# Optimization experiments

Measured on AMD Instinct MI355X. Metric: run time of the kernel, lower is better.

Reference implementation:

```python
import jax, jax.numpy as jnp
import numpy as np

EPS = 1e-12
FP8_MAX = 448.0  # torch.finfo(float8_e4m3fn).max
G = 128  # tile/block group size


def per_tile_quant_dequant(x):
    # x: [seq, din]; one scale per 1x128 tile along din (per_tile_quant semantics)
    s, d = x.shape
    xt = x.reshape(s, d // G, G)
    amax = jnp.max(jnp.abs(xt), axis=-1, keepdims=True)
    scale = jnp.maximum(amax, EPS) / FP8_MAX
    q = jnp.clip(xt / scale, -FP8_MAX, FP8_MAX).astype(jnp.float8_e4m3fn)
    return (q.astype(jnp.float32) * scale).reshape(s, d)


def per_block_quant_dequant(w):
    # w: [ne, dout, din]; one scale per 128x128 block
    ne, dout, din = w.shape
    wb = w.reshape(ne, dout // G, G, din // G, G)
    amax = jnp.max(jnp.abs(wb), axis=(2, 4), keepdims=True)
    scale = jnp.maximum(amax, EPS) / FP8_MAX
    q = jnp.clip(wb / scale, -FP8_MAX, FP8_MAX).astype(jnp.float8_e4m3fn)
    return (q.astype(jnp.float32) * scale).reshape(ne, dout, din)


def grouped_gemm(xq, wq, tokens_per_expert):
    # xq: [seq, din] (tokens contiguous per expert); wq: [ne, dout, din]
    seq = xq.shape[0]
    ne, dout, _ = wq.shape
    ends = jnp.cumsum(tokens_per_expert)
    starts = ends - tokens_per_expert
    tok = jnp.arange(seq)
    out = jnp.zeros((seq, dout), dtype=jnp.float32)
    for e in range(ne):  # small fixed expert count
        mask = ((tok >= starts[e]) & (tok < ends[e]))[:, None]
        xe = jnp.where(mask, xq, 0.0)
        out = out + xe @ wq[e].T
    return out


def setup_inputs() -> dict:
    key = jax.random.key(0)
    k1, k2 = jax.random.split(key)
    ne, dout, din, seq = 8, 2048, 2048, 8192
    x = jax.random.normal(k1, (seq, din), dtype=jnp.float32)
    # weight stored flat as (ne*dout, din), as in the module
    weight = jax.random.normal(k2, (ne * dout, din), dtype=jnp.float32) * 0.02
    tokens_per_expert = jnp.full((ne,), seq // ne, dtype=jnp.int32)
    return {"input": x, "weight": weight, "tokens_per_expert": tokens_per_expert}


def reference(input, weight, tokens_per_expert):
    ne, dout, din = 8, 2048, 2048
    w = weight.reshape(ne, dout, din)
    xq = per_tile_quant_dequant(input)          # per-tile fp8 activation quant
    wq = per_block_quant_dequant(w)             # per-block fp8 weight quant
    return grouped_gemm(xq, wq, tokens_per_expert)
```

## Files before the change

kernel.cpp:

```cpp
#include <hip/hip_runtime.h>
#include <hip/hip_bf16.h>
#include <stdint.h>

#define NE   8
#define DOUT 2048
#define DIN  2048
#define SEQ  8192
#define GSZ  128
#define FP8_MAX 448.0f
#define EPSQ 1e-12f

typedef float f32x4  __attribute__((ext_vector_type(4)));
typedef float f32x16 __attribute__((ext_vector_type(16)));
typedef int   i32x4  __attribute__((ext_vector_type(4)));
typedef int   i32x8  __attribute__((ext_vector_type(8)));

__device__ __forceinline__ void async16(void* lds_base, const void* gptr) {
    __builtin_amdgcn_global_load_lds(
        (const __attribute__((address_space(1))) unsigned int*)gptr,
        (__attribute__((address_space(3))) unsigned int*)lds_base,
        16, 0, 0);
}

__global__ __launch_bounds__(256) void quant_x_kernel(
    const float* __restrict__ x, unsigned char* __restrict__ qx,
    float* __restrict__ sx)
{
    const int g = blockIdx.x * 256 + threadIdx.x;
    const float4 v = ((const float4*)x)[g];
    float a = fmaxf(fmaxf(fabsf(v.x), fabsf(v.y)),
                    fmaxf(fabsf(v.z), fabsf(v.w)));
    #pragma unroll
    for (int o = 16; o; o >>= 1) a = fmaxf(a, __shfl_xor(a, o));
    const float scale = fmaxf(a, EPSQ) / FP8_MAX;
    const int tile = g >> 5;
    if ((threadIdx.x & 31) == 0) sx[tile] = scale;

    float q0 = fminf(fmaxf(v.x / scale, -FP8_MAX), FP8_MAX);
    float q1 = fminf(fmaxf(v.y / scale, -FP8_MAX), FP8_MAX);
    float q2 = fminf(fmaxf(v.z / scale, -FP8_MAX), FP8_MAX);
    float q3 = fminf(fmaxf(v.w / scale, -FP8_MAX), FP8_MAX);
    int lo = __builtin_amdgcn_cvt_pk_fp8_f32(q0, q1, 0, false);
    int pk = __builtin_amdgcn_cvt_pk_fp8_f32(q2, q3, lo, true);
    ((unsigned int*)qx)[g] = (unsigned int)pk;
}

__global__ __launch_bounds__(256) void quant_w_kernel(
    const float* __restrict__ w, unsigned char* __restrict__ qw,
    float* __restrict__ sw)
{
    __shared__ float buf[128 * 128];
    __shared__ float red[4];

    const int cb = blockIdx.x;
    const int rb = blockIdx.y;
    const int e  = blockIdx.z;
    const int t  = threadIdx.x;
    const int lane = t & 63, wv = t >> 6;

    const size_t base = ((size_t)e * DOUT + rb * GSZ) * DIN + cb * GSZ;
    const float* wp = w + base;

    #pragma unroll
    for (int j = 0; j < 16; ++j) {
        int f16 = (wv * 16 + j) * 64 + lane;
        int row = f16 >> 5, cc = f16 & 31;
        async16(buf + (wv * 16 + j) * 256,
                wp + (size_t)row * DIN + cc * 4);
    }
    __syncthreads();

    float a = 0.f;
    #pragma unroll
    for (int i = 0; i < 16; ++i) {
        f32x4 v = *(const f32x4*)(buf + (t + i * 256) * 4);
        a = fmaxf(a, fmaxf(fmaxf(fabsf(v[0]), fabsf(v[1])),
                           fmaxf(fabsf(v[2]), fabsf(v[3]))));
    }
    #pragma unroll
    for (int o = 32; o; o >>= 1) a = fmaxf(a, __shfl_xor(a, o));
    if (lane == 0) red[wv] = a;
    __syncthreads();
    a = fmaxf(fmaxf(red[0], red[1]), fmaxf(red[2], red[3]));
    const float scale = fmaxf(a, EPSQ) / FP8_MAX;
    if (t == 0) sw[(e * 16 + rb) * 16 + cb] = scale;

    unsigned int* qout = (unsigned int*)(qw + base);
    #pragma unroll
    for (int i = 0; i < 16; ++i) {
        int idx = t + i * 256;
        f32x4 v = *(const f32x4*)(buf + idx * 4);
        float q0 = fminf(fmaxf(v[0] / scale, -FP8_MAX), FP8_MAX);
        float q1 = fminf(fmaxf(v[1] / scale, -FP8_MAX), FP8_MAX);
        float q2 = fminf(fmaxf(v[2] / scale, -FP8_MAX), FP8_MAX);
        float q3 = fminf(fmaxf(v[3] / scale, -FP8_MAX), FP8_MAX);
        int lo = __builtin_amdgcn_cvt_pk_fp8_f32(q0, q1, 0, false);
        int pk = __builtin_amdgcn_cvt_pk_fp8_f32(q2, q3, lo, true);
        int r = idx >> 5, c4 = idx & 31;
        qout[r * (DIN / 4) + c4] = (unsigned int)pk;
    }
}

__global__ __launch_bounds__(512, 2) void gemm_kernel(
    const unsigned char* __restrict__ qx, const float* __restrict__ sx,
    const unsigned char* __restrict__ qw, const float* __restrict__ sw,
    const int* __restrict__ tpe, float* __restrict__ out)
{
    __shared__ __align__(16) unsigned char Asm[2][256 * 128];
    __shared__ __align__(16) unsigned char Bsm[2][256 * 128];
    __shared__ __align__(16) float Rs[16 * 256];
    __shared__ __align__(16) float SwL[2 * 16];

    const int tid  = threadIdx.x;
    const int lane = tid & 63;
    const int wv   = tid >> 6;
    const int wm   = wv >> 2;
    const int wn   = wv & 3;
    const int l31  = lane & 31;
    const int h    = lane >> 5;
    const int nh   = wn >> 1;

    const int lid  = blockIdx.x;
    const int xcd  = lid & 7, t8 = lid >> 3;
    const int mbid = xcd * 4 + (t8 >> 3);
    const int nb   = t8 & 7;
    const int r0   = mbid * 256, n0 = nb * 256;

    int e = -1, start = 0;
    #pragma unroll
    for (int i = 0; i < NE; ++i) {
        int end = start + tpe[i];
        if (r0 >= start && r0 < end) e = i;
        start = end;
    }
    if (e < 0) {
        f32x4 z = {0.f, 0.f, 0.f, 0.f};
        for (int i = tid; i < 256 * 64; i += 512) {
            int r = i >> 6, c4 = i & 63;
            *(f32x4*)(out + (size_t)(r0 + r) * DOUT + n0 + c4 * 4) = z;
        }
        return;
    }

    for (int i = tid; i < 16 * 256; i += 512) {
        int row = i >> 4, kb = i & 15;
        const float* sp = sx + (size_t)(r0 + row) * 16;
        Rs[kb * 256 + row] = (kb == 0) ? sp[15] : sp[kb - 1] / sp[kb];
    }
    if (tid < 32) {
        int nhh = tid >> 4, kb = tid & 15;
        const float* wp = sw + ((e * 16) + (nb * 2 + nhh)) * 16;
        SwL[nhh * 16 + kb] = (kb == 0) ? wp[15] : wp[kb - 1] / wp[kb];
    }

    const unsigned char* Ag = qx + (size_t)r0 * DIN;
    const unsigned char* Bg = qw + (size_t)e * DOUT * DIN + (size_t)n0 * DIN;

    int soff[4], ldst[4];
    #pragma unroll
    for (int j = 0; j < 4; ++j) {
        int f = wv * 4096 + j * 1024 + lane * 16;
        int row = f >> 7, pc = (f >> 4) & 7;
        soff[j] = row * DIN + ((pc ^ (row & 7)) * 16);
        ldst[j] = wv * 4096 + j * 1024;
    }

    int abase[4], ax8[4], bbase[2], bx8[2];
    #pragma unroll
    for (int mi = 0; mi < 4; ++mi) {
        int ra = wm * 128 + mi * 32 + l31;
        abase[mi] = ra * 128; ax8[mi] = ra & 7;
    }
    #pragma unroll
    for (int ni = 0; ni < 2; ++ni) {
        int rb = wn * 64 + ni * 32 + l31;
        bbase[ni] = rb * 128; bx8[ni] = rb & 7;
    }

    #pragma unroll
    for (int j = 0; j < 4; ++j) {
        async16(Asm[0] + ldst[j], Ag + soff[j]);
        async16(Bsm[0] + ldst[j], Bg + soff[j]);
    }
    asm volatile("s_waitcnt lgkmcnt(0)" ::: "memory");

    f32x16 acc[4][2];
    #pragma unroll
    for (int mi = 0; mi < 4; ++mi)
        #pragma unroll
        for (int ni = 0; ni < 2; ++ni)
            #pragma unroll
            for (int q = 0; q < 16; ++q) acc[mi][ni][q] = 0.f;

    for (int kb = 0; kb < 16; ++kb) {
        const unsigned char* Ac = Asm[kb & 1];
        const unsigned char* Bc = Bsm[kb & 1];
        unsigned char* An = Asm[(kb & 1) ^ 1];
        unsigned char* Bn = Bsm[(kb & 1) ^ 1];
        float rwk = 1.f;
        i32x8 Bf[2][2];

        #pragma unroll
        for (int p = 0; p < 4; ++p) {
            if (kb < 15) {
                async16(An + ldst[p], Ag + soff[p] + (kb + 1) * GSZ);
                async16(Bn + ldst[p], Bg + soff[p] + (kb + 1) * GSZ);
            }
            if (p == 0) {
                if (kb < 15) asm volatile("s_waitcnt vmcnt(2)" ::: "memory");
                else         asm volatile("s_waitcnt vmcnt(0)" ::: "memory");
                __builtin_amdgcn_s_barrier();
                asm volatile("" ::: "memory");
            }
            if (p == 0) {
                #pragma unroll
                for (int ks = 0; ks < 2; ++ks) {
                    const int c0 = ks * 4 + h * 2;
                    #pragma unroll
                    for (int ni = 0; ni < 2; ++ni) {
                        i32x4 lo = *(const i32x4*)(Bc + bbase[ni] + (((c0    ) ^ bx8[ni]) * 16));
                        i32x4 hi = *(const i32x4*)(Bc + bbase[ni] + (((c0 + 1) ^ bx8[ni]) * 16));
                        #pragma unroll
                        for (int q = 0; q < 4; ++q) {
                            Bf[ks][ni][q] = lo[q]; Bf[ks][ni][q + 4] = hi[q];
                        }
                    }
                }
                rwk = SwL[nh * 16 + kb];
            }
            i32x8 Af[2];
            #pragma unroll
            for (int ks = 0; ks < 2; ++ks) {
                const int c0 = ks * 4 + h * 2;
                i32x4 lo = *(const i32x4*)(Ac + abase[p] + (((c0    ) ^ ax8[p]) * 16));
                i32x4 hi = *(const i32x4*)(Ac + abase[p] + (((c0 + 1) ^ ax8[p]) * 16));
                #pragma unroll
                for (int q = 0; q < 4; ++q) { Af[ks][q] = lo[q]; Af[ks][q + 4] = hi[q]; }
            }
            f32x4 rr[4];
            if (kb) {
                const float* rp = Rs + kb * 256 + wm * 128 + p * 32 + 4 * h;
                #pragma unroll
                for (int g = 0; g < 4; ++g) {
                    f32x4 t = *(const f32x4*)(rp + 8 * g);
                    rr[g] = t * rwk;
                }
            }

            __builtin_amdgcn_s_barrier();
            __builtin_amdgcn_s_setprio(1);
            if (kb) {
                #pragma unroll
                for (int ni = 0; ni < 2; ++ni)
                    #pragma unroll
                    for (int g = 0; g < 4; ++g)
                        #pragma unroll
                        for (int j = 0; j < 4; ++j)
                            acc[p][ni][g * 4 + j] *= rr[g][j];
            }
            #pragma unroll
            for (int ks = 0; ks < 2; ++ks)
                #pragma unroll
                for (int ni = 0; ni < 2; ++ni)
                    acc[p][ni] = __builtin_amdgcn_mfma_scale_f32_32x32x64_f8f6f4(
                        Af[ks], Bf[ks][ni], acc[p][ni],
                        0, 0,
                        0, 0x7f7f7f7f,
                        0, 0x7f7f7f7f);
            __builtin_amdgcn_s_setprio(0);
            __builtin_amdgcn_s_barrier();
        }
    }

    const float fw = SwL[nh * 16 + 0];
    #pragma unroll
    for (int mi = 0; mi < 4; ++mi) {
        const float* fp = Rs + wm * 128 + mi * 32 + 4 * h;
        f32x4 fv[4];
        #pragma unroll
        for (int g = 0; g < 4; ++g) {
            f32x4 t = *(const f32x4*)(fp + 8 * g);
            fv[g] = t * fw;
        }
        const int rbase = r0 + wm * 128 + mi * 32 + 4 * h;
        #pragma unroll
        for (int ni = 0; ni < 2; ++ni) {
            const int col = n0 + wn * 64 + ni * 32 + l31;
            #pragma unroll
            for (int g = 0; g < 4; ++g)
                #pragma unroll
                for (int j = 0; j < 4; ++j)
                    out[(size_t)(rbase + 8 * g + j) * DOUT + col] =
                        acc[mi][ni][g * 4 + j] * fv[g][j];
        }
    }
}

extern "C" void kernel_launch(void* const* d_in, const int* in_sizes, int n_in,
                              void* d_out, int out_size, void* d_ws, size_t ws_size,
                              hipStream_t stream) {
    const float* x   = (const float*)d_in[0];
    const float* wt  = (const float*)d_in[1];
    const int*   tpe = (const int*)d_in[2];
    float* out = (float*)d_out;

    char* ws = (char*)d_ws;
    unsigned char* qx = (unsigned char*)ws;
    unsigned char* qw = qx + (size_t)SEQ * DIN;
    float* sx = (float*)(qw + (size_t)NE * DOUT * DIN);
    float* sw = sx + (size_t)SEQ * 16;

    quant_x_kernel<<<SEQ * DIN / 4 / 256, 256, 0, stream>>>(x, qx, sx);
    quant_w_kernel<<<dim3(16, 16, NE), 256, 0, stream>>>(wt, qw, sw);
    gemm_kernel<<<256, 512, 0, stream>>>(qx, sx, qw, sw, tpe, out);
}
```

Baseline: 322.9 us.

## Collapse per-subtile phases into one barrier-synchronized compute block per K step

The K loop no longer splits into four sub-phases, each with its own async loads, LDS fragment reads, accumulator rescale and s_barrier pair. All eight prefetch loads for the next K tile are now issued up front and followed by a single vmcnt wait and barrier. After that, every accumulator is rescaled at once and the MFMAs run with the ks loop outermost. The aim is to cut barrier count and phase overhead per K block. In exchange, global-load issue is no longer interleaved with the MFMA sub-phases, and the coarser grouping may change register pressure and scheduling.

```diff
diff --git a/kernel.cpp b/kernel.cpp
--- a/kernel.cpp
+++ b/kernel.cpp
@@ -195,81 +195,75 @@
     for (int kb = 0; kb < 16; ++kb) {
         const unsigned char* Ac = Asm[kb & 1];
         const unsigned char* Bc = Bsm[kb & 1];
-        unsigned char* An = Asm[(kb & 1) ^ 1];
-        unsigned char* Bn = Bsm[(kb & 1) ^ 1];
-        float rwk = 1.f;
-        i32x8 Bf[2][2];
-
-        #pragma unroll
-        for (int p = 0; p < 4; ++p) {
-            if (kb < 15) {
-                async16(An + ldst[p], Ag + soff[p] + (kb + 1) * GSZ);
-                async16(Bn + ldst[p], Bg + soff[p] + (kb + 1) * GSZ);
+
+        if (kb < 15) {
+            unsigned char* An = Asm[(kb & 1) ^ 1];
+            unsigned char* Bn = Bsm[(kb & 1) ^ 1];
+            #pragma unroll
+            for (int j = 0; j < 4; ++j) {
+                async16(An + ldst[j], Ag + soff[j] + (kb + 1) * GSZ);
+                async16(Bn + ldst[j], Bg + soff[j] + (kb + 1) * GSZ);
             }
-            if (p == 0) {
-                if (kb < 15) asm volatile("s_waitcnt vmcnt(2)" ::: "memory");
-                else         asm volatile("s_waitcnt vmcnt(0)" ::: "memory");
-                __builtin_amdgcn_s_barrier();
-                asm volatile("" ::: "memory");
-            }
-            if (p == 0) {
-                #pragma unroll
-                for (int ks = 0; ks < 2; ++ks) {
-                    const int c0 = ks * 4 + h * 2;
-                    #pragma unroll
-                    for (int ni = 0; ni < 2; ++ni) {
-                        i32x4 lo = *(const i32x4*)(Bc + bbase[ni] + (((c0    ) ^ bx8[ni]) * 16));
-                        i32x4 hi = *(const i32x4*)(Bc + bbase[ni] + (((c0 + 1) ^ bx8[ni]) * 16));
-                        #pragma unroll
-                        for (int q = 0; q < 4; ++q) {
-                            Bf[ks][ni][q] = lo[q]; Bf[ks][ni][q + 4] = hi[q];
-                        }
-                    }
-                }
-                rwk = SwL[nh * 16 + kb];
-            }
-            i32x8 Af[2];
-            #pragma unroll
-            for (int ks = 0; ks < 2; ++ks) {
-                const int c0 = ks * 4 + h * 2;
-                i32x4 lo = *(const i32x4*)(Ac + abase[p] + (((c0    ) ^ ax8[p]) * 16));
-                i32x4 hi = *(const i32x4*)(Ac + abase[p] + (((c0 + 1) ^ ax8[p]) * 16));
-                #pragma unroll
-                for (int q = 0; q < 4; ++q) { Af[ks][q] = lo[q]; Af[ks][q + 4] = hi[q]; }
-            }
-            f32x4 rr[4];
-            if (kb) {
-                const float* rp = Rs + kb * 256 + wm * 128 + p * 32 + 4 * h;
+            asm volatile("s_waitcnt vmcnt(8)" ::: "memory");
+        } else {
+            asm volatile("s_waitcnt vmcnt(0)" ::: "memory");
+        }
+        __builtin_amdgcn_s_barrier();
+        asm volatile("" ::: "memory");
+
+        if (kb) {
+            const float rwk = SwL[nh * 16 + kb];
+            #pragma unroll
+            for (int mi = 0; mi < 4; ++mi) {
+                const float* rp = Rs + kb * 256 + wm * 128 + mi * 32 + 4 * h;
+                f32x4 rr[4];
                 #pragma unroll
                 for (int g = 0; g < 4; ++g) {
                     f32x4 t = *(const f32x4*)(rp + 8 * g);
                     rr[g] = t * rwk;
                 }
-            }
-
-            __builtin_amdgcn_s_barrier();
-            __builtin_amdgcn_s_setprio(1);
-            if (kb) {
                 #pragma unroll
                 for (int ni = 0; ni < 2; ++ni)
                     #pragma unroll
                     for (int g = 0; g < 4; ++g)
                         #pragma unroll
                         for (int j = 0; j < 4; ++j)
-                            acc[p][ni][g * 4 + j] *= rr[g][j];
+                            acc[mi][ni][g * 4 + j] *= rr[g][j];
             }
-            #pragma unroll
-            for (int ks = 0; ks < 2; ++ks)
+        }
+
+        __builtin_amdgcn_s_setprio(1);
+        #pragma unroll
+        for (int ks = 0; ks < 2; ++ks) {
+            const int c0 = ks * 4 + h * 2;
+            i32x8 Bf[2];
+            #pragma unroll
+            for (int ni = 0; ni < 2; ++ni) {
+                i32x4 lo = *(const i32x4*)(Bc + bbase[ni] + (((c0    ) ^ bx8[ni]) * 16));
+                i32x4 hi = *(const i32x4*)(Bc + bbase[ni] + (((c0 + 1) ^ bx8[ni]) * 16));
+                #pragma unroll
+                for (int q = 0; q < 4; ++q) { Bf[ni][q] = lo[q]; Bf[ni][q + 4] = hi[q]; }
+            }
+            #pragma unroll
+            for (int mi = 0; mi < 4; ++mi) {
+                i32x8 Af;
+                i32x4 alo = *(const i32x4*)(Ac + abase[mi] + (((c0    ) ^ ax8[mi]) * 16));
+                i32x4 ahi = *(const i32x4*)(Ac + abase[mi] + (((c0 + 1) ^ ax8[mi]) * 16));
+                #pragma unroll
+                for (int q = 0; q < 4; ++q) { Af[q] = alo[q]; Af[q + 4] = ahi[q]; }
                 #pragma unroll
                 for (int ni = 0; ni < 2; ++ni)
-                    acc[p][ni] = __builtin_amdgcn_mfma_scale_f32_32x32x64_f8f6f4(
-                        Af[ks], Bf[ks][ni], acc[p][ni],
+                    acc[mi][ni] = __builtin_amdgcn_mfma_scale_f32_32x32x64_f8f6f4(
+                        Af, Bf[ni], acc[mi][ni],
                         0, 0,
                         0, 0x7f7f7f7f,
                         0, 0x7f7f7f7f);
-            __builtin_amdgcn_s_setprio(0);
-            __builtin_amdgcn_s_barrier();
-        }
+            }
+        }
+        __builtin_amdgcn_s_setprio(0);
+        asm volatile("" ::: "memory");
+        __builtin_amdgcn_s_barrier();
+        asm volatile("" ::: "memory");
     }
 
     const float fw = SwL[nh * 16 + 0];
```

Measured after the change: 302.4 us. 6.4% less time.
